# Kernel tuning notes

Measured on AMD Instinct MI355X. Metric: run time of the kernel, lower is better.

Reference implementation:

```python
import jax, jax.numpy as jnp
import numpy as np
from jax import lax

N = 4096
INPUT_SIZE = 2048
HIDDEN = 256
HEADS = 4
T_POWER = 6
K_KNN = 30   # N >= 300 branch in compute_markov_tensor_optic
KA = 10      # int(k/3)


def setup_inputs() -> dict:
    key = jax.random.key(0)
    k1, k2, k3, k4, k5 = jax.random.split(key, 5)
    bound = 1.0 / np.sqrt(INPUT_SIZE)
    return {
        "input_tensor": jax.random.normal(k1, (N, INPUT_SIZE), dtype=jnp.float32),
        "Wq": jax.random.uniform(k2, (HEADS, HIDDEN, INPUT_SIZE), jnp.float32, -bound, bound),
        "bq": jax.random.uniform(k3, (HEADS, HIDDEN), jnp.float32, -bound, bound),
        "Wk": jax.random.uniform(k4, (HEADS, HIDDEN, INPUT_SIZE), jnp.float32, -bound, bound),
        "bk": jax.random.uniform(k5, (HEADS, HIDDEN), jnp.float32, -bound, bound),
    }


def _markov(q, k):
    # q, k: [N, HIDDEN]; pairwise Euclidean distances via gram trick
    sq = (jnp.sum(q * q, axis=1)[:, None]
          + jnp.sum(k * k, axis=1)[None, :]
          - 2.0 * (q @ k.T))
    d = jnp.sqrt(jnp.maximum(sq, 0.0) + 1e-10)          # [N, N]
    # adaptive bandwidth: (KA)-th smallest distance per row
    md = jnp.sort(d, axis=1)[:, KA]                      # [N]
    d = d / (md[:, None] + 1e-10)
    aff = jnp.exp(-(d ** 2))                             # epsilon = 1
    # knn pruning: keep entries >= k-th largest per row
    kth = lax.top_k(aff, K_KNN)[0][:, -1]                # [N]
    aff = aff * (aff >= kth[:, None]).astype(aff.dtype)
    idx = jnp.arange(aff.shape[0])
    aff = aff.at[idx, idx].set(1.0)
    return aff + aff.T


def reference(input_tensor, Wq, bq, Wk, bk):
    # per-head projections: [HEADS, N, HIDDEN]
    q = jnp.einsum('nd,hkd->hnk', input_tensor, Wq) + bq[:, None, :]
    k = jnp.einsum('nd,hkd->hnk', input_tensor, Wk) + bk[:, None, :]
    aff = jax.vmap(_markov)(q, k)                        # [HEADS, N, N]
    probs = jax.nn.softmax(aff, axis=-1)
    probs_t = jnp.linalg.matrix_power(probs, T_POWER)    # batched matrix power
    ctx = jnp.einsum('hnm,md->hnd', probs_t, input_tensor)  # [HEADS, N, INPUT_SIZE]
    return jnp.mean(ctx, axis=0)
```

## Files before the change

### kernel.cpp

```cpp
#include <hip/hip_runtime.h>
#include <hip/hip_bf16.h>
#include <math.h>

#define NN 4096
#define DIN 2048
#define HID 256
#define NHEADS 4
#define CAP 1024
#define OVF_CAP 131072
#define PW 128

__global__ __launch_bounds__(256) void proj_kernel(
    const float* __restrict__ X, const float* __restrict__ Wq, const float* __restrict__ bq,
    const float* __restrict__ Wk, const float* __restrict__ bk,
    float* __restrict__ qb, float* __restrict__ kb, int h0)
{
    const int isK  = blockIdx.z & 1;
    const int hidx = blockIdx.z >> 1;
    const int hh   = h0 + hidx;
    const float* W    = (isK ? Wk : Wq) + (size_t)hh * HID * DIN;
    const float* bias = (isK ? bk : bq) + hh * HID;
    float* out = (isK ? kb : qb) + (size_t)hidx * NN * HID;

    const int bm = blockIdx.x * 64;
    const int bn = blockIdx.y * 64;
    const int t  = threadIdx.x;
    const int tx = t & 15, ty = t >> 4;
    const int lr = t >> 2, lk = (t & 3) * 4;

    __shared__ float As[16][68];
    __shared__ float Bs[16][68];
    float acc[4][4] = {};

    for (int k0 = 0; k0 < DIN; k0 += 16) {
        float4 av = *(const float4*)(X + (size_t)(bm + lr) * DIN + k0 + lk);
        float4 bv = *(const float4*)(W + (size_t)(bn + lr) * DIN + k0 + lk);
        As[lk+0][lr]=av.x; As[lk+1][lr]=av.y; As[lk+2][lr]=av.z; As[lk+3][lr]=av.w;
        Bs[lk+0][lr]=bv.x; Bs[lk+1][lr]=bv.y; Bs[lk+2][lr]=bv.z; Bs[lk+3][lr]=bv.w;
        __syncthreads();
        #pragma unroll
        for (int kk = 0; kk < 16; ++kk) {
            const float4 a4 = *(const float4*)&As[kk][ty*4];
            const float4 b4 = *(const float4*)&Bs[kk][tx*4];
            const float a[4] = {a4.x,a4.y,a4.z,a4.w};
            const float b[4] = {b4.x,b4.y,b4.z,b4.w};
            #pragma unroll
            for (int i = 0; i < 4; ++i)
                #pragma unroll
                for (int j = 0; j < 4; ++j)
                    acc[i][j] = fmaf(a[i], b[j], acc[i][j]);
        }
        __syncthreads();
    }
    #pragma unroll
    for (int i = 0; i < 4; ++i) {
        const int m = bm + ty*4 + i;
        float4 o;
        o.x = acc[i][0] + bias[bn+tx*4+0];
        o.y = acc[i][1] + bias[bn+tx*4+1];
        o.z = acc[i][2] + bias[bn+tx*4+2];
        o.w = acc[i][3] + bias[bn+tx*4+3];
        *(float4*)(out + (size_t)m * HID + bn + tx*4) = o;
    }
}

__global__ __launch_bounds__(64) void rownorm_kernel(
    const float* __restrict__ q, const float* __restrict__ k,
    float* __restrict__ sqq, float* __restrict__ sqk)
{
    const int row = blockIdx.x;
    const int hz  = blockIdx.z;
    const int lane = threadIdx.x;
    const float* src = (blockIdx.y ? k : q) + ((size_t)hz * NN + row) * HID;
    float4 v = *(const float4*)(src + lane * 4);
    float s = v.x*v.x + v.y*v.y + v.z*v.z + v.w*v.w;
    for (int off = 32; off; off >>= 1) s += __shfl_down(s, off);
    if (lane == 0) (blockIdx.y ? sqk : sqq)[(size_t)hz * NN + row] = s;
}

__global__ __launch_bounds__(256) void dist_kernel(
    const float* __restrict__ q, const float* __restrict__ k,
    const float* __restrict__ sqq, const float* __restrict__ sqk,
    float* __restrict__ Dm)
{
    const int bm = blockIdx.x * 64;
    const int bn = blockIdx.y * 64;
    const int t  = threadIdx.x;
    const int tx = t & 15, ty = t >> 4;
    const int lr = t >> 2, lk = (t & 3) * 4;

    __shared__ float As[16][68];
    __shared__ float Bs[16][68];
    float acc[4][4] = {};

    for (int k0 = 0; k0 < HID; k0 += 16) {
        float4 av = *(const float4*)(q + (size_t)(bm + lr) * HID + k0 + lk);
        float4 bv = *(const float4*)(k + (size_t)(bn + lr) * HID + k0 + lk);
        As[lk+0][lr]=av.x; As[lk+1][lr]=av.y; As[lk+2][lr]=av.z; As[lk+3][lr]=av.w;
        Bs[lk+0][lr]=bv.x; Bs[lk+1][lr]=bv.y; Bs[lk+2][lr]=bv.z; Bs[lk+3][lr]=bv.w;
        __syncthreads();
        #pragma unroll
        for (int kk = 0; kk < 16; ++kk) {
            const float4 a4 = *(const float4*)&As[kk][ty*4];
            const float4 b4 = *(const float4*)&Bs[kk][tx*4];
            const float a[4] = {a4.x,a4.y,a4.z,a4.w};
            const float b[4] = {b4.x,b4.y,b4.z,b4.w};
            #pragma unroll
            for (int i = 0; i < 4; ++i)
                #pragma unroll
                for (int j = 0; j < 4; ++j)
                    acc[i][j] = fmaf(a[i], b[j], acc[i][j]);
        }
        __syncthreads();
    }
    #pragma unroll
    for (int i = 0; i < 4; ++i) {
        const int m = bm + ty*4 + i;
        const float sm = sqq[m];
        float4 o;
        float v0 = sm + sqk[bn+tx*4+0] - 2.0f*acc[i][0];
        float v1 = sm + sqk[bn+tx*4+1] - 2.0f*acc[i][1];
        float v2 = sm + sqk[bn+tx*4+2] - 2.0f*acc[i][2];
        float v3 = sm + sqk[bn+tx*4+3] - 2.0f*acc[i][3];
        o.x = sqrtf(fmaxf(v0, 0.0f) + 1e-10f);
        o.y = sqrtf(fmaxf(v1, 0.0f) + 1e-10f);
        o.z = sqrtf(fmaxf(v2, 0.0f) + 1e-10f);
        o.w = sqrtf(fmaxf(v3, 0.0f) + 1e-10f);
        *(float4*)(Dm + (size_t)m * NN + bn + tx*4) = o;
    }
}

__device__ __forceinline__ unsigned kth_reg(const unsigned (&r)[64], int K)
{
    unsigned lo = 0u, hi = 0xFFFFFFFFu;
    while (lo < hi) {
        unsigned mid = lo + ((hi - lo) >> 1);
        int c = 0;
        #pragma unroll
        for (int i = 0; i < 64; ++i)
            c += (int)__popcll(__ballot(r[i] <= mid));
        if (c >= K) hi = mid; else lo = mid + 1;
    }
    return lo;
}

__global__ __launch_bounds__(64) void select_kernel(
    const float* __restrict__ Dm, float* __restrict__ mdp, float* __restrict__ kth)
{
    const int row = blockIdx.x;
    const int lane = threadIdx.x;
    const float* src = Dm + (size_t)row * NN + lane * 64;
    unsigned r[64];
    #pragma unroll
    for (int c = 0; c < 16; ++c) {
        float4 v = *(const float4*)(src + c * 4);
        r[c*4+0] = __float_as_uint(v.x);
        r[c*4+1] = __float_as_uint(v.y);
        r[c*4+2] = __float_as_uint(v.z);
        r[c*4+3] = __float_as_uint(v.w);
    }
    unsigned v11 = kth_reg(r, 11);
    unsigned v30 = kth_reg(r, 30);
    if (lane == 0) {
        float md = __uint_as_float(v11) + 1e-10f;
        float t  = __uint_as_float(v30) / md;
        mdp[row] = md;
        kth[row] = expf(-(t*t));
    }
}

__device__ __forceinline__ void aff4(float4& v, float m, float kt, bool diagtile,
                                     int r, int lc4)
{
    float t0 = v.x / m, t1 = v.y / m, t2 = v.z / m, t3 = v.w / m;
    float a0 = expf(-(t0*t0)), a1 = expf(-(t1*t1)), a2 = expf(-(t2*t2)), a3 = expf(-(t3*t3));
    a0 = (a0 >= kt) ? a0 : 0.0f;
    a1 = (a1 >= kt) ? a1 : 0.0f;
    a2 = (a2 >= kt) ? a2 : 0.0f;
    a3 = (a3 >= kt) ? a3 : 0.0f;
    if (diagtile) {
        if (lc4+0 == r) a0 = 1.0f;
        if (lc4+1 == r) a1 = 1.0f;
        if (lc4+2 == r) a2 = 1.0f;
        if (lc4+3 == r) a3 = 1.0f;
    }
    v.x = a0; v.y = a1; v.z = a2; v.w = a3;
}

__global__ __launch_bounds__(256) void affsym_kernel(
    float* __restrict__ Dm, const float* __restrict__ mdp, const float* __restrict__ kthv,
    int* __restrict__ ovf_cnt)
{
    if (blockIdx.x == 0 && threadIdx.x == 0) *ovf_cnt = 0;

    int rem = blockIdx.x;
    int bi = 0;
    while (rem >= 64 - bi) { rem -= 64 - bi; ++bi; }
    const int bj = bi + rem;
    const bool diagtile = (bi == bj);

    __shared__ float T1[64][65];
    __shared__ float T2[64][65];
    const int t = threadIdx.x;
    const int lr = t >> 4;
    const int lc4 = (t & 15) * 4;

    #pragma unroll
    for (int rr = 0; rr < 4; ++rr) {
        const int r = rr*16 + lr;
        {
            const int grow = bi*64 + r;
            const float m  = mdp[grow];
            const float kt = kthv[grow];
            float4 v1 = *(const float4*)(Dm + (size_t)grow * NN + bj*64 + lc4);
            aff4(v1, m, kt, diagtile, r, lc4);
            T1[r][lc4+0]=v1.x; T1[r][lc4+1]=v1.y; T1[r][lc4+2]=v1.z; T1[r][lc4+3]=v1.w;
        }
        {
            const int grow = bj*64 + r;
            const float m  = mdp[grow];
            const float kt = kthv[grow];
            float4 v2 = *(const float4*)(Dm + (size_t)grow * NN + bi*64 + lc4);
            aff4(v2, m, kt, diagtile, r, lc4);
            T2[r][lc4+0]=v2.x; T2[r][lc4+1]=v2.y; T2[r][lc4+2]=v2.z; T2[r][lc4+3]=v2.w;
        }
    }
    __syncthreads();
    #pragma unroll
    for (int rr = 0; rr < 4; ++rr) {
        const int r = rr*16 + lr;
        float4 o1;
        o1.x = T1[r][lc4+0] + T2[lc4+0][r];
        o1.y = T1[r][lc4+1] + T2[lc4+1][r];
        o1.z = T1[r][lc4+2] + T2[lc4+2][r];
        o1.w = T1[r][lc4+3] + T2[lc4+3][r];
        *(float4*)(Dm + (size_t)(bi*64 + r) * NN + bj*64 + lc4) = o1;
        if (!diagtile) {
            float4 o2;
            o2.x = T2[r][lc4+0] + T1[lc4+0][r];
            o2.y = T2[r][lc4+1] + T1[lc4+1][r];
            o2.z = T2[r][lc4+2] + T1[lc4+2][r];
            o2.w = T2[r][lc4+3] + T1[lc4+3][r];
            *(float4*)(Dm + (size_t)(bj*64 + r) * NN + bi*64 + lc4) = o2;
        }
    }
}

__global__ __launch_bounds__(256) void stats_extract_kernel(
    const float* __restrict__ A, float* __restrict__ cvec, int* __restrict__ nnz,
    int* __restrict__ cols, float* __restrict__ vals,
    int* __restrict__ ovf_cnt, int* __restrict__ ovf_row,
    int* __restrict__ ovf_col, float* __restrict__ ovf_val)
{
    __shared__ float srow[NN];
    __shared__ float red[8];
    __shared__ int cnt;
    const int row = blockIdx.x, t = threadIdx.x;
    const int lane = t & 63, wid = t >> 6;
    const float* src = A + (size_t)row * NN;

    float mx = -1e30f;
    #pragma unroll
    for (int c = 0; c < 4; ++c) {
        const int base = c*1024 + t*4;
        float4 v = *(const float4*)(src + base);
        *(float4*)&srow[base] = v;
        mx = fmaxf(mx, fmaxf(fmaxf(v.x, v.y), fmaxf(v.z, v.w)));
    }
    for (int off = 32; off; off >>= 1) mx = fmaxf(mx, __shfl_xor(mx, off));
    if (lane == 0) red[wid] = mx;
    __syncthreads();
    mx = fmaxf(fmaxf(red[0], red[1]), fmaxf(red[2], red[3]));

    float sum = 0.0f;
    #pragma unroll
    for (int c = 0; c < 4; ++c) {
        const int base = c*1024 + t*4;
        float4 v = *(float4*)&srow[base];
        sum += expf(v.x-mx) + expf(v.y-mx) + expf(v.z-mx) + expf(v.w-mx);
    }
    for (int off = 32; off; off >>= 1) sum += __shfl_xor(sum, off);
    if (lane == 0) red[4 + wid] = sum;
    if (t == 0) cnt = 0;
    __syncthreads();
    sum = red[4] + red[5] + red[6] + red[7];
    const float ci = expf(-mx) / sum;
    if (t == 0) cvec[row] = ci;

    for (int c = 0; c < 16; ++c) {
        const int j = c*256 + t;
        const float a = srow[j];
        if (a != 0.0f) {
            const float v = expf(a - mx)/sum - ci;
            int p = atomicAdd(&cnt, 1);
            if (p < CAP) {
                cols[(size_t)row*CAP + p] = j;
                vals[(size_t)row*CAP + p] = v;
            } else {
                int q = atomicAdd(ovf_cnt, 1);
                if (q < OVF_CAP) {
                    ovf_row[q] = row;
                    ovf_col[q] = j;
                    ovf_val[q] = v;
                }
            }
        }
    }
    __syncthreads();
    if (t == 0) {
        const int c2 = min(cnt, CAP);
        const int e2 = min((c2 + 7) & ~7, CAP);
        for (int p = c2; p < e2; ++p) {
            cols[(size_t)row*CAP + p] = 0;
            vals[(size_t)row*CAP + p] = 0.0f;
        }
        nnz[row] = e2 == c2 ? c2 : e2;
    }
}

__global__ __launch_bounds__(256) void colsum_partial_kernel(
    const float* __restrict__ Y, float* __restrict__ part)
{
    const int cc = blockIdx.y * 256 + threadIdx.x;
    const int r0 = blockIdx.x * 128;
    float s = 0.0f;
    for (int r = 0; r < 128; ++r) s += Y[(size_t)(r0 + r) * DIN + cc];
    part[(size_t)blockIdx.x * DIN + cc] = s;
}

__global__ __launch_bounds__(256) void colsum_final_kernel(
    const float* __restrict__ part, float* __restrict__ colsum)
{
    const int cc = blockIdx.x * 256 + threadIdx.x;
    float s = 0.0f;
    #pragma unroll
    for (int r = 0; r < 32; ++r) s += part[(size_t)r * DIN + cc];
    colsum[cc] = s;
}

typedef float vf4 __attribute__((ext_vector_type(4)));

#define SPMM_LOAD(buf, b)                                               \
    _Pragma("unroll")                                                   \
    for (int u = 0; u < 4; ++u) {                                       \
        const int j = half ? rc[(b) + 2*u + 1] : rc[(b) + 2*u];         \
        buf[u] = *(const float4*)(Y + (size_t)j * DIN + cq);            \
    }

#define SPMM_FMA(buf, b)                                                \
    _Pragma("unroll")                                                   \
    for (int u = 0; u < 4; ++u) {                                       \
        const float v = half ? rv[(b) + 2*u + 1] : rv[(b) + 2*u];       \
        ax = fmaf(v, buf[u].x, ax);                                     \
        ay = fmaf(v, buf[u].y, ay);                                     \
        az = fmaf(v, buf[u].z, az);                                     \
        aw = fmaf(v, buf[u].w, aw);                                     \
    }

__global__ __launch_bounds__(256) void spmm_kernel(
    const float* __restrict__ Y, const float* __restrict__ colsum,
    const float* __restrict__ cvec, const int* __restrict__ nnz,
    const int* __restrict__ cols, const float* __restrict__ vals,
    float* __restrict__ Yout, int mode)
{
    const int wave = threadIdx.x >> 6, lane = threadIdx.x & 63;
    const int half = lane >> 5;
    const int qc   = (lane & 31) * 4;

    const int id     = blockIdx.x;
    const int xcd    = id & 7;
    const int w      = id >> 3;
    const int panel  = xcd + ((w & 1024) ? 8 : 0);
    const int rowblk = w & 1023;

    const int row = __builtin_amdgcn_readfirstlane(rowblk * 4 + wave);
    const int cq  = panel * PW + qc;

    const int n = nnz[row];
    const float ci = cvec[row];
    const int*   rc = cols + (size_t)row * CAP;
    const float* rv = vals + (size_t)row * CAP;

    const float4 s = *(const float4*)(colsum + cq);
    float ax = half ? 0.0f : ci * s.x;
    float ay = half ? 0.0f : ci * s.y;
    float az = half ? 0.0f : ci * s.z;
    float aw = half ? 0.0f : ci * s.w;

    float4 yA[4], yB[4];
    SPMM_LOAD(yA, 0);
    int base = 8;
    bool tailA = true;
    while (base < n) {
        SPMM_LOAD(yB, base);
        SPMM_FMA(yA, base - 8);
        base += 8;
        if (base < n) {
            SPMM_LOAD(yA, base);
            SPMM_FMA(yB, base - 8);
            base += 8;
        } else {
            SPMM_FMA(yB, base - 8);
            tailA = false;
            break;
        }
    }
    if (tailA) { SPMM_FMA(yA, base - 8); }

    ax += __shfl_xor(ax, 32);
    ay += __shfl_xor(ay, 32);
    az += __shfl_xor(az, 32);
    aw += __shfl_xor(aw, 32);

    if (half == 0) {
        float* dst = Yout + (size_t)row * DIN + cq;
        vf4 o;
        if (mode == 0)      { o[0] = ax;       o[1] = ay;       o[2] = az;       o[3] = aw; }
        else if (mode == 1) { o[0] = 0.25f*ax; o[1] = 0.25f*ay; o[2] = 0.25f*az; o[3] = 0.25f*aw; }
        else {
            const vf4 p = __builtin_nontemporal_load((const vf4*)dst);
            o[0] = p[0] + 0.25f*ax; o[1] = p[1] + 0.25f*ay;
            o[2] = p[2] + 0.25f*az; o[3] = p[3] + 0.25f*aw;
        }
        __builtin_nontemporal_store(o, (vf4*)dst);
    }
}

__global__ __launch_bounds__(256) void spmm_fixup_kernel(
    const float* __restrict__ Y, const int* __restrict__ ovf_cnt,
    const int* __restrict__ ovf_row, const int* __restrict__ ovf_col,
    const float* __restrict__ ovf_val, float* __restrict__ Yout, float scale)
{
    const int cnt = min(*ovf_cnt, OVF_CAP);
    const int t = threadIdx.x;
    for (int e = blockIdx.x; e < cnt; e += gridDim.x) {
        const int i = ovf_row[e], j = ovf_col[e];
        const float v = ovf_val[e] * scale;
        const float* yr = Y + (size_t)j * DIN;
        float* dst = Yout + (size_t)i * DIN;
        #pragma unroll
        for (int c = t*4; c < DIN; c += 1024) {
            atomicAdd(dst + c + 0, v * yr[c + 0]);
            atomicAdd(dst + c + 1, v * yr[c + 1]);
            atomicAdd(dst + c + 2, v * yr[c + 2]);
            atomicAdd(dst + c + 3, v * yr[c + 3]);
        }
    }
}

extern "C" void kernel_launch(void* const* d_in, const int* in_sizes, int n_in,
                              void* d_out, int out_size, void* d_ws, size_t ws_size,
                              hipStream_t stream)
{
    const float* X  = (const float*)d_in[0];
    const float* Wq = (const float*)d_in[1];
    const float* bq = (const float*)d_in[2];
    const float* Wk = (const float*)d_in[3];
    const float* bk = (const float*)d_in[4];
    float* out = (float*)d_out;

    const size_t nf_batched = 8ull*NN*HID + (size_t)NN*NN + 2ull*(size_t)NN*CAP
                            + 32ull*DIN + 2ull*DIN + 8ull*NN
                            + 3ull*NN  + (size_t)NN
                            + 16 + 3ull*OVF_CAP;
    const bool batched = ws_size >= nf_batched * sizeof(float);
    const int nhq = batched ? NHEADS : 1;

    float* ws    = (float*)d_ws;
    float* qbufs = ws;
    float* kbufs = qbufs + (size_t)nhq*NN*HID;
    float* A     = kbufs + (size_t)nhq*NN*HID;
    float* Y1    = A;
    float* Y2    = A + (size_t)NN*DIN;
    float* valsA = A + (size_t)NN*NN;
    int*   colsA = (int*)(valsA + (size_t)NN*CAP);
    float* part  = (float*)(colsA + (size_t)NN*CAP);
    float* colsumX = part + 32*DIN;
    float* colsumB = colsumX + DIN;
    float* sqq  = colsumB + DIN;
    float* sqk  = sqq + (size_t)nhq*NN;
    float* mdp  = sqk + (size_t)nhq*NN;
    float* kth  = mdp + NN;
    float* cvec = kth + NN;
    int*   nnz  = (int*)(cvec + NN);
    int*   ovf_cnt = nnz + NN;
    int*   ovf_row = ovf_cnt + 16;
    int*   ovf_col = ovf_row + OVF_CAP;
    float* ovf_val = (float*)(ovf_col + OVF_CAP);

    if (batched) {
        proj_kernel<<<dim3(NN/64, HID/64, 2*NHEADS), 256, 0, stream>>>(
            X, Wq, bq, Wk, bk, qbufs, kbufs, 0);
        rownorm_kernel<<<dim3(NN, 2, NHEADS), 64, 0, stream>>>(qbufs, kbufs, sqq, sqk);
    }
    colsum_partial_kernel<<<dim3(32, DIN/256), 256, 0, stream>>>(X, part);
    colsum_final_kernel<<<dim3(DIN/256), 256, 0, stream>>>(part, colsumX);

    for (int h = 0; h < NHEADS; ++h) {
        if (!batched) {
            proj_kernel<<<dim3(NN/64, HID/64, 2), 256, 0, stream>>>(
                X, Wq, bq, Wk, bk, qbufs, kbufs, h);
            rownorm_kernel<<<dim3(NN, 2, 1), 64, 0, stream>>>(qbufs, kbufs, sqq, sqk);
        }
        const size_t ho = batched ? (size_t)h : 0;
        const float* qh   = qbufs + ho * NN * HID;
        const float* kh   = kbufs + ho * NN * HID;
        const float* sqqh = sqq + ho * NN;
        const float* sqkh = sqk + ho * NN;

        dist_kernel<<<dim3(NN/64, NN/64), 256, 0, stream>>>(qh, kh, sqqh, sqkh, A);
        select_kernel<<<dim3(NN), 64, 0, stream>>>(A, mdp, kth);
        affsym_kernel<<<dim3(2080), 256, 0, stream>>>(A, mdp, kth, ovf_cnt);
        stats_extract_kernel<<<dim3(NN), 256, 0, stream>>>(A, cvec, nnz, colsA, valsA,
                                                           ovf_cnt, ovf_row, ovf_col, ovf_val);

        const float* src = X;
        for (int tpow = 1; tpow <= 6; ++tpow) {
            const float* cs;
            if (tpow == 1) {
                cs = colsumX;
            } else {
                colsum_partial_kernel<<<dim3(32, DIN/256), 256, 0, stream>>>(src, part);
                colsum_final_kernel<<<dim3(DIN/256), 256, 0, stream>>>(part, colsumB);
                cs = colsumB;
            }
            float* dst;
            int mode;
            if (tpow == 6)      { dst = out; mode = (h == 0) ? 1 : 2; }
            else if (tpow & 1)  { dst = Y1;  mode = 0; }
            else                { dst = Y2;  mode = 0; }
            spmm_kernel<<<dim3((NN/4) * (DIN/PW)), 256, 0, stream>>>(src, cs, cvec, nnz, colsA, valsA, dst, mode);
            spmm_fixup_kernel<<<dim3(64), 256, 0, stream>>>(src, ovf_cnt, ovf_row, ovf_col, ovf_val,
                                                            dst, (tpow == 6) ? 0.25f : 1.0f);
            src = dst;
        }
    }
}
```

Baseline: 6.129 ms.

## Fuse overflow fixup and column-sum accumulation into the SpMM kernel

The separate atomic overflow fixup kernel is removed. Each SpMM wave now scans the overflow list and adds the entries for its own row before storing. The column sums of each intermediate Y are also accumulated with atomics into 32 partial slots in the SpMM epilogue, so the colsum pass no longer re-reads the full 4096x2048 matrix each power step. A small drain kernel reduces the partials and re-zeroes them. The cost is millions of contended float atomics per step, plus a serial scan of the overflow list in every wave, which gets expensive if overflow is non-empty.

```diff
diff --git a/kernel.cpp b/kernel.cpp
--- a/kernel.cpp
+++ b/kernel.cpp
@@ -338,6 +338,19 @@
     colsum[cc] = s;
 }
 
+__global__ __launch_bounds__(256) void colsum_drain_kernel(
+    float* __restrict__ part, float* __restrict__ colsum)
+{
+    const int c = blockIdx.x * 256 + threadIdx.x;
+    float s = 0.0f;
+    #pragma unroll
+    for (int r = 0; r < 32; ++r) {
+        s += part[(size_t)r * DIN + c];
+        part[(size_t)r * DIN + c] = 0.0f;
+    }
+    colsum[c] = s;
+}
+
 typedef float vf4 __attribute__((ext_vector_type(4)));
 
 #define SPMM_LOAD(buf, b)                                               \
@@ -361,7 +374,10 @@
     const float* __restrict__ Y, const float* __restrict__ colsum,
     const float* __restrict__ cvec, const int* __restrict__ nnz,
     const int* __restrict__ cols, const float* __restrict__ vals,
-    float* __restrict__ Yout, int mode)
+    float* __restrict__ Yout, int mode,
+    const int* __restrict__ ovf_cnt, const int* __restrict__ ovf_row,
+    const int* __restrict__ ovf_col, const float* __restrict__ ovf_val,
+    float* __restrict__ part, int do_part)
 {
     const int wave = threadIdx.x >> 6, lane = threadIdx.x & 63;
     const int half = lane >> 5;
@@ -412,6 +428,21 @@
     az += __shfl_xor(az, 32);
     aw += __shfl_xor(aw, 32);
 
+    const int ocnt = min(*ovf_cnt, OVF_CAP);
+    for (int e = 0; e < ocnt; ++e) {
+        if (ovf_row[e] == row) {
+            const int j = ovf_col[e];
+            const float v = ovf_val[e];
+            if (half == 0) {
+                const float4 yv = *(const float4*)(Y + (size_t)j * DIN + cq);
+                ax = fmaf(v, yv.x, ax);
+                ay = fmaf(v, yv.y, ay);
+                az = fmaf(v, yv.z, az);
+                aw = fmaf(v, yv.w, aw);
+            }
+        }
+    }
+
     if (half == 0) {
         float* dst = Yout + (size_t)row * DIN + cq;
         vf4 o;
@@ -423,27 +454,13 @@
             o[2] = p[2] + 0.25f*az; o[3] = p[3] + 0.25f*aw;
         }
         __builtin_nontemporal_store(o, (vf4*)dst);
-    }
-}
-
-__global__ __launch_bounds__(256) void spmm_fixup_kernel(
-    const float* __restrict__ Y, const int* __restrict__ ovf_cnt,
-    const int* __restrict__ ovf_row, const int* __restrict__ ovf_col,
-    const float* __restrict__ ovf_val, float* __restrict__ Yout, float scale)
-{
-    const int cnt = min(*ovf_cnt, OVF_CAP);
-    const int t = threadIdx.x;
-    for (int e = blockIdx.x; e < cnt; e += gridDim.x) {
-        const int i = ovf_row[e], j = ovf_col[e];
-        const float v = ovf_val[e] * scale;
-        const float* yr = Y + (size_t)j * DIN;
-        float* dst = Yout + (size_t)i * DIN;
-        #pragma unroll
-        for (int c = t*4; c < DIN; c += 1024) {
-            atomicAdd(dst + c + 0, v * yr[c + 0]);
-            atomicAdd(dst + c + 1, v * yr[c + 1]);
-            atomicAdd(dst + c + 2, v * yr[c + 2]);
-            atomicAdd(dst + c + 3, v * yr[c + 3]);
+
+        if (do_part) {
+            float* pp = part + (size_t)(rowblk & 31) * DIN + cq;
+            atomicAdd(pp + 0, o[0]);
+            atomicAdd(pp + 1, o[1]);
+            atomicAdd(pp + 2, o[2]);
+            atomicAdd(pp + 3, o[3]);
         }
     }
 }
@@ -495,6 +512,7 @@
     }
     colsum_partial_kernel<<<dim3(32, DIN/256), 256, 0, stream>>>(X, part);
     colsum_final_kernel<<<dim3(DIN/256), 256, 0, stream>>>(part, colsumX);
+    hipMemsetAsync(part, 0, 32ull * DIN * sizeof(float), stream);
 
     for (int h = 0; h < NHEADS; ++h) {
         if (!batched) {
@@ -520,8 +538,7 @@
             if (tpow == 1) {
                 cs = colsumX;
             } else {
-                colsum_partial_kernel<<<dim3(32, DIN/256), 256, 0, stream>>>(src, part);
-                colsum_final_kernel<<<dim3(DIN/256), 256, 0, stream>>>(part, colsumB);
+                colsum_drain_kernel<<<dim3(DIN/256), 256, 0, stream>>>(part, colsumB);
                 cs = colsumB;
             }
             float* dst;
@@ -529,9 +546,10 @@
             if (tpow == 6)      { dst = out; mode = (h == 0) ? 1 : 2; }
             else if (tpow & 1)  { dst = Y1;  mode = 0; }
             else                { dst = Y2;  mode = 0; }
-            spmm_kernel<<<dim3((NN/4) * (DIN/PW)), 256, 0, stream>>>(src, cs, cvec, nnz, colsA, valsA, dst, mode);
-            spmm_fixup_kernel<<<dim3(64), 256, 0, stream>>>(src, ovf_cnt, ovf_row, ovf_col, ovf_val,
-                                                            dst, (tpow == 6) ? 0.25f : 1.0f);
+            const int do_part = (tpow < 6) ? 1 : 0;
+            spmm_kernel<<<dim3((NN/4) * (DIN/PW)), 256, 0, stream>>>(
+                src, cs, cvec, nnz, colsA, valsA, dst, mode,
+                ovf_cnt, ovf_row, ovf_col, ovf_val, part, do_part);
             src = dst;
         }
     }
```

New measurement: 16.36 ms. 2.67x slower.
